# Kernel optimization log

Measured on AMD Instinct MI355X. Metric: run time of the kernel, lower is better.

The kernel has to match this reference:

```python
import jax, jax.numpy as jnp
import numpy as np

HIP_L, HIP_R = 11, 12          # hip joint indices along V
K_LIST = (2, 3, 4, 5)          # soft-selector kNN MoE k values
TAU = 0.35                     # tau_center for ball softmax
EPS = 1e-6


def _sym_norm(A):
    # D^{-1/2} A D^{-1/2} without materializing diag matrices
    d = A.sum(-1)
    dis = jax.lax.rsqrt(d + EPS)
    return dis[..., :, None] * A * dis[..., None, :]


def _knn_adj(pos, k):
    # pos: (N, M, 3) -> 0/1 kNN adjacency (+I self loop, diag ends up 2 as in torch ref)
    M = pos.shape[1]
    diff = pos[:, :, None, :] - pos[:, None, :, :]
    d = jnp.sqrt(jnp.sum(diff * diff, axis=-1))  # (N, M, M) euclidean cdist
    idx = jax.lax.top_k(-d, k)[1]                # (N, M, k) k smallest distances (incl. self)
    A = jax.nn.one_hot(idx, M, dtype=pos.dtype).sum(2)  # scatter 1.0 at kNN columns
    return A + jnp.eye(M, dtype=pos.dtype)


def setup_inputs() -> dict:
    key = jax.random.key(0)
    k1, k2 = jax.random.split(key)
    N, C, T, V, M = 64, 8, 300, 17, 12
    x = jax.random.normal(k1, (N, C, T, V, M), jnp.float32)
    alpha_logits = jax.random.normal(k2, (len(K_LIST),), jnp.float32) * 0.1
    lambda_fuse = jnp.array([0.1], jnp.float32)
    tag_gate = jnp.array([1.0], jnp.float32)
    return {"x": x, "alpha_logits": alpha_logits,
            "lambda_fuse": lambda_fuse, "tag_gate": tag_gate}


def reference(x, alpha_logits, lambda_fuse, tag_gate):
    N, C, T, V, M = x.shape
    # hip-root position averaged over time: (N, M, 3)
    root3 = 0.5 * (x[:, 0:3, :, HIP_L, :] + x[:, 0:3, :, HIP_R, :])  # (N,3,T,M)
    pos = root3.mean(2).transpose(0, 2, 1)                           # (N,M,3)

    # kNN mixture-of-graphs, sym-normalized, detached (detach_adj=True)
    A_knn_stack = jnp.stack([_sym_norm(_knn_adj(pos, k)) for k in K_LIST], 1)  # (N,K,M,M)
    A_knn_stack = jax.lax.stop_gradient(A_knn_stack)
    alpha = jax.nn.softmax(alpha_logits)          # global selector, temp=1
    A_knn = jnp.einsum('k,nkij->nij', alpha, A_knn_stack)

    # soft ball-star graph
    s = x[:, 3].mean((1, 2))                      # (N,M) ball score
    p = jax.nn.softmax(s / TAU, axis=1)
    A_ball = p[:, :, None] + p[:, None, :] + jnp.eye(M, dtype=x.dtype)
    A_ball = jax.lax.stop_gradient(_sym_norm(A_ball))

    # adaptive ball weight from confidence of p (NOT detached)
    w = jnp.clip((jnp.max(p, 1, keepdims=True) - 1.0 / M) / (1.0 - 1.0 / M + EPS), 0.0, 1.0)
    A = w[:, :, None] * A_ball + (1.0 - w[:, :, None]) * A_knn  # (N,M,M)

    # message passing across persons on hip-root features, fused back residually
    root = 0.5 * (x[:, :, :, HIP_L, :] + x[:, :, :, HIP_R, :])  # (N,C,T,M)
    agg = jnp.einsum('nuv,nctv->nctu', A, root)                 # (N,C,T,M)
    g = jnp.tanh(tag_gate[0])  # ramp=1 (ramp_epochs=0), gate_max=1
    return x + g * lambda_fuse[0] * (agg - root)[:, :, :, None, :]
```

## Files before the change

### kernel.cpp

```cpp
#include <hip/hip_runtime.h>
#include <math.h>

#define N_ 64
#define C_ 8
#define T_ 300
#define V_ 17
#define M_ 12
#define EPSF 1e-6f
#define TAUF 0.35f


#define TSPLIT 10
#define TCH (T_ / TSPLIT)

__global__ __launch_bounds__(256) void k_reduce(const float* __restrict__ x,
                                                float* __restrict__ ws_pos,
                                                float* __restrict__ ws_s) {
    const int n = blockIdx.x;
    const int t0 = blockIdx.y * TCH;
    const int tid = threadIdx.x;
    __shared__ float pos_acc[36];
    __shared__ float s_acc[12];
    if (tid < 36) pos_acc[tid] = 0.f;
    if (tid < 12) s_acc[tid] = 0.f;
    __syncthreads();

    {
        const float* xs = x + ((size_t)(n * C_ + 3) * T_ + t0) * 204;
        float a0 = 0.f, a1 = 0.f, a2 = 0.f;
        for (int e = tid; e < TCH * 204; e += 768) {
            a0 += xs[e];
            if (e + 256 < TCH * 204) a1 += xs[e + 256];
            if (e + 512 < TCH * 204) a2 += xs[e + 512];
        }
        int m0 = tid % 12;
        atomicAdd(&s_acc[m0], a0);
        atomicAdd(&s_acc[(m0 + 4) % 12], a1);
        atomicAdd(&s_acc[(m0 + 8) % 12], a2);
    }

    for (int e = tid; e < 3 * TCH * 24; e += 256) {
        int d = e / (TCH * 24);
        int rem = e % (TCH * 24);
        int tt = rem / 24, j = rem % 24;
        float val = x[((size_t)(n * C_ + d) * T_ + t0 + tt) * 204 + 132 + j];
        atomicAdd(&pos_acc[d * 12 + (j % 12)], val);
    }
    __syncthreads();

    if (tid < 36) atomicAdd(&ws_pos[n * 36 + tid], pos_acc[tid]);
    if (tid < 12) atomicAdd(&ws_s[n * 12 + tid], s_acc[tid]);
}

__global__ __launch_bounds__(64) void k_adj(const float* __restrict__ ws_pos,
                                            const float* __restrict__ ws_s,
                                            const float* __restrict__ alpha_logits,
                                            float* __restrict__ ws_A) {
    const int n = blockIdx.x;
    const int tid = threadIdx.x;
    __shared__ float posx[12], posy[12], posz[12];
    __shared__ float dist[144];
    __shared__ int ord[60];
    __shared__ float p_s[12];
    __shared__ float alpha_s[4];
    __shared__ float w_s;

    const float PSC = 0.5f / (float)T_;
    if (tid < 12) {
        posx[tid] = ws_pos[n * 36 + 0 * 12 + tid] * PSC;
        posy[tid] = ws_pos[n * 36 + 1 * 12 + tid] * PSC;
        posz[tid] = ws_pos[n * 36 + 2 * 12 + tid] * PSC;
    }
    if (tid == 0) {
        float l0 = alpha_logits[0], l1 = alpha_logits[1], l2 = alpha_logits[2], l3 = alpha_logits[3];
        float mx = fmaxf(fmaxf(l0, l1), fmaxf(l2, l3));
        float e0 = expf(l0 - mx), e1 = expf(l1 - mx), e2 = expf(l2 - mx), e3 = expf(l3 - mx);
        float s = e0 + e1 + e2 + e3;
        alpha_s[0] = e0 / s; alpha_s[1] = e1 / s; alpha_s[2] = e2 / s; alpha_s[3] = e3 / s;
    }
    if (tid == 1) {
        const float SSC = 1.f / (float)(T_ * V_);
        float sv[12];
        float mx = -1e30f;
        #pragma unroll
        for (int m = 0; m < 12; ++m) { sv[m] = (ws_s[n * 12 + m] * SSC) * (1.f / TAUF); mx = fmaxf(mx, sv[m]); }
        float sum = 0.f;
        #pragma unroll
        for (int m = 0; m < 12; ++m) { sv[m] = expf(sv[m] - mx); sum += sv[m]; }
        float maxp = 0.f;
        #pragma unroll
        for (int m = 0; m < 12; ++m) { sv[m] = sv[m] / sum; p_s[m] = sv[m]; maxp = fmaxf(maxp, sv[m]); }
        float w = (maxp - 1.f / 12.f) / (1.f - 1.f / 12.f + EPSF);
        w_s = fminf(fmaxf(w, 0.f), 1.f);
    }
    __syncthreads();

    for (int e = tid; e < 144; e += 64) {
        int i = e / 12, j = e % 12;
        float dx = posx[i] - posx[j], dy = posy[i] - posy[j], dz = posz[i] - posz[j];
        dist[e] = sqrtf(dx * dx + dy * dy + dz * dz);
    }
    __syncthreads();

    if (tid < 12) {
        int i = tid, mask = 0;
        #pragma unroll
        for (int r = 0; r < 5; ++r) {
            float bd = 1e30f; int bj = -1;
            #pragma unroll
            for (int j = 0; j < 12; ++j) {
                if (!((mask >> j) & 1)) {
                    float dd = dist[i * 12 + j];
                    if (dd < bd) { bd = dd; bj = j; }
                }
            }
            ord[i * 5 + r] = bj; mask |= (1 << bj);
        }
    }
    __syncthreads();

    float w = w_s;
    for (int e = tid; e < 144; e += 64) {
        int i = e / 12, j = e % 12;
        int rank = 5;
        #pragma unroll
        for (int r = 4; r >= 0; --r) if (ord[i * 5 + r] == j) rank = r;
        float diag = (i == j) ? 1.f : 0.f;
        float aknn = 0.f;
        #pragma unroll
        for (int kk = 0; kk < 4; ++kk) {
            int K = kk + 2;
            float val = ((rank < K) ? 1.f : 0.f) + diag;
            aknn += alpha_s[kk] * val / ((float)(K + 1) + EPSF);
        }
        float pi = p_s[i], pj = p_s[j];
        float di = 12.f * pi + 2.f, dj = 12.f * pj + 2.f;
        float ab = (pi + pj + diag) * rsqrtf(di + EPSF) * rsqrtf(dj + EPSF);
        ws_A[n * 144 + e] = w * ab + (1.f - w) * aknn;
    }
}

#define RT 30
__global__ __launch_bounds__(256) void k_main(const float* __restrict__ x,
                                              const float* __restrict__ ws_A,
                                              const float* __restrict__ lambda_fuse,
                                              const float* __restrict__ tag_gate,
                                              float* __restrict__ out) {
    const int n = blockIdx.y;
    const int r0 = blockIdx.x * RT;
    const int tid = threadIdx.x;
    __shared__ float Ash[144];
    __shared__ float root_sh[RT * 12];
    __shared__ float delta_sh[RT * 12];

    if (tid < 144) Ash[tid] = ws_A[n * 144 + tid];
    float scale = tanhf(tag_gate[0]) * lambda_fuse[0];

    const float* xn = x + (size_t)n * 2400 * 204;
    float* on = out + (size_t)n * 2400 * 204;

    for (int e = tid; e < RT * 12; e += 256) {
        int r = e / 12, v = e % 12;
        const float* row = xn + (size_t)(r0 + r) * 204;
        root_sh[e] = 0.5f * (row[132 + v] + row[144 + v]);
    }
    __syncthreads();
    for (int e = tid; e < RT * 12; e += 256) {
        int r = e / 12, u = e % 12;
        float acc = 0.f;
        #pragma unroll
        for (int v = 0; v < 12; ++v) acc += Ash[u * 12 + v] * root_sh[r * 12 + v];
        delta_sh[e] = scale * (acc - root_sh[e]);
    }
    __syncthreads();

    const float4* x4 = (const float4*)(xn + (size_t)r0 * 204);
    float4* o4 = (float4*)(on + (size_t)r0 * 204);
    for (int f = tid; f < RT * 51; f += 256) {
        int r = f / 51, j = f % 51;
        int m0 = (4 * j) % 12;
        float4 v = x4[(size_t)r * 51 + j];
        const float* d = &delta_sh[r * 12 + m0];
        v.x += d[0]; v.y += d[1]; v.z += d[2]; v.w += d[3];
        o4[(size_t)r * 51 + j] = v;
    }
}

extern "C" void kernel_launch(void* const* d_in, const int* in_sizes, int n_in,
                              void* d_out, int out_size, void* d_ws, size_t ws_size,
                              hipStream_t stream) {
    const float* x = (const float*)d_in[0];
    const float* alpha_logits = (const float*)d_in[1];
    const float* lambda_fuse = (const float*)d_in[2];
    const float* tag_gate = (const float*)d_in[3];
    float* out = (float*)d_out;

    float* ws = (float*)d_ws;
    float* ws_pos = ws;
    float* ws_s = ws + 64 * 36;
    float* ws_A = ws + 64 * 48;

    hipMemsetAsync(ws, 0, (size_t)(64 * 48) * sizeof(float), stream);

    k_reduce<<<dim3(N_, TSPLIT), dim3(256), 0, stream>>>(x, ws_pos, ws_s);
    k_adj<<<dim3(N_), dim3(64), 0, stream>>>(ws_pos, ws_s, alpha_logits, ws_A);
    k_main<<<dim3(2400 / RT, N_), dim3(256), 0, stream>>>(x, ws_A, lambda_fuse, tag_gate, out);
}
```

Measured before the change: 255.6 us.

## Drop memset via per-block partial slots; stage x tile in LDS with nontemporal stores

Result: no change. 250.8 us (-1.9%).

```diff
diff --git a/kernel.cpp b/kernel.cpp
--- a/kernel.cpp
+++ b/kernel.cpp
@@ -9,15 +9,17 @@
 #define EPSF 1e-6f
 #define TAUF 0.35f
 
+typedef float f32x4 __attribute__((ext_vector_type(4)));
+
 
 #define TSPLIT 10
 #define TCH (T_ / TSPLIT)
 
 __global__ __launch_bounds__(256) void k_reduce(const float* __restrict__ x,
-                                                float* __restrict__ ws_pos,
-                                                float* __restrict__ ws_s) {
+                                                float* __restrict__ ws_part) {
     const int n = blockIdx.x;
-    const int t0 = blockIdx.y * TCH;
+    const int by = blockIdx.y;
+    const int t0 = by * TCH;
     const int tid = threadIdx.x;
     __shared__ float pos_acc[36];
     __shared__ float s_acc[12];
@@ -48,16 +50,17 @@
     }
     __syncthreads();
 
-    if (tid < 36) atomicAdd(&ws_pos[n * 36 + tid], pos_acc[tid]);
-    if (tid < 12) atomicAdd(&ws_s[n * 12 + tid], s_acc[tid]);
-}
-
-__global__ __launch_bounds__(64) void k_adj(const float* __restrict__ ws_pos,
-                                            const float* __restrict__ ws_s,
+    float* slot = ws_part + (size_t)(n * TSPLIT + by) * 48;
+    if (tid < 36) slot[tid] = pos_acc[tid];
+    if (tid < 12) slot[36 + tid] = s_acc[tid];
+}
+
+__global__ __launch_bounds__(64) void k_adj(const float* __restrict__ ws_part,
                                             const float* __restrict__ alpha_logits,
                                             float* __restrict__ ws_A) {
     const int n = blockIdx.x;
     const int tid = threadIdx.x;
+    __shared__ float raw[48];
     __shared__ float posx[12], posy[12], posz[12];
     __shared__ float dist[144];
     __shared__ int ord[60];
@@ -65,11 +68,19 @@
     __shared__ float alpha_s[4];
     __shared__ float w_s;
 
+    if (tid < 48) {
+        float a = 0.f;
+        #pragma unroll
+        for (int j = 0; j < TSPLIT; ++j) a += ws_part[(size_t)(n * TSPLIT + j) * 48 + tid];
+        raw[tid] = a;
+    }
+    __syncthreads();
+
     const float PSC = 0.5f / (float)T_;
     if (tid < 12) {
-        posx[tid] = ws_pos[n * 36 + 0 * 12 + tid] * PSC;
-        posy[tid] = ws_pos[n * 36 + 1 * 12 + tid] * PSC;
-        posz[tid] = ws_pos[n * 36 + 2 * 12 + tid] * PSC;
+        posx[tid] = raw[0 * 12 + tid] * PSC;
+        posy[tid] = raw[1 * 12 + tid] * PSC;
+        posz[tid] = raw[2 * 12 + tid] * PSC;
     }
     if (tid == 0) {
         float l0 = alpha_logits[0], l1 = alpha_logits[1], l2 = alpha_logits[2], l3 = alpha_logits[3];
@@ -79,11 +90,11 @@
         alpha_s[0] = e0 / s; alpha_s[1] = e1 / s; alpha_s[2] = e2 / s; alpha_s[3] = e3 / s;
     }
     if (tid == 1) {
-        const float SSC = 1.f / (float)(T_ * V_);
+        const float SSC = 1.f / ((float)(T_ * V_) * TAUF);
         float sv[12];
         float mx = -1e30f;
         #pragma unroll
-        for (int m = 0; m < 12; ++m) { sv[m] = (ws_s[n * 12 + m] * SSC) * (1.f / TAUF); mx = fmaxf(mx, sv[m]); }
+        for (int m = 0; m < 12; ++m) { sv[m] = raw[36 + m] * SSC; mx = fmaxf(mx, sv[m]); }
         float sum = 0.f;
         #pragma unroll
         for (int m = 0; m < 12; ++m) { sv[m] = expf(sv[m] - mx); sum += sv[m]; }
@@ -149,20 +160,26 @@
     const int n = blockIdx.y;
     const int r0 = blockIdx.x * RT;
     const int tid = threadIdx.x;
+    __shared__ f32x4 xs4[RT * 51];
     __shared__ float Ash[144];
     __shared__ float root_sh[RT * 12];
     __shared__ float delta_sh[RT * 12];
+    float* xs = (float*)xs4;
 
     if (tid < 144) Ash[tid] = ws_A[n * 144 + tid];
     float scale = tanhf(tag_gate[0]) * lambda_fuse[0];
 
     const float* xn = x + (size_t)n * 2400 * 204;
     float* on = out + (size_t)n * 2400 * 204;
+    const f32x4* x4 = (const f32x4*)(xn + (size_t)r0 * 204);
+    f32x4* o4 = (f32x4*)(on + (size_t)r0 * 204);
+
+    for (int f = tid; f < RT * 51; f += 256) xs4[f] = x4[f];
+    __syncthreads();
 
     for (int e = tid; e < RT * 12; e += 256) {
         int r = e / 12, v = e % 12;
-        const float* row = xn + (size_t)(r0 + r) * 204;
-        root_sh[e] = 0.5f * (row[132 + v] + row[144 + v]);
+        root_sh[e] = 0.5f * (xs[r * 204 + 132 + v] + xs[r * 204 + 144 + v]);
     }
     __syncthreads();
     for (int e = tid; e < RT * 12; e += 256) {
@@ -174,15 +191,13 @@
     }
     __syncthreads();
 
-    const float4* x4 = (const float4*)(xn + (size_t)r0 * 204);
-    float4* o4 = (float4*)(on + (size_t)r0 * 204);
     for (int f = tid; f < RT * 51; f += 256) {
         int r = f / 51, j = f % 51;
         int m0 = (4 * j) % 12;
-        float4 v = x4[(size_t)r * 51 + j];
+        f32x4 v = xs4[f];
         const float* d = &delta_sh[r * 12 + m0];
         v.x += d[0]; v.y += d[1]; v.z += d[2]; v.w += d[3];
-        o4[(size_t)r * 51 + j] = v;
+        __builtin_nontemporal_store(v, &o4[f]);
     }
 }
 
@@ -196,13 +211,10 @@
     float* out = (float*)d_out;
 
     float* ws = (float*)d_ws;
-    float* ws_pos = ws;
-    float* ws_s = ws + 64 * 36;
-    float* ws_A = ws + 64 * 48;
-
-    hipMemsetAsync(ws, 0, (size_t)(64 * 48) * sizeof(float), stream);
-
-    k_reduce<<<dim3(N_, TSPLIT), dim3(256), 0, stream>>>(x, ws_pos, ws_s);
-    k_adj<<<dim3(N_), dim3(64), 0, stream>>>(ws_pos, ws_s, alpha_logits, ws_A);
+    float* ws_part = ws;
+    float* ws_A = ws + 64 * TSPLIT * 48;
+
+    k_reduce<<<dim3(N_, TSPLIT), dim3(256), 0, stream>>>(x, ws_part);
+    k_adj<<<dim3(N_), dim3(64), 0, stream>>>(ws_part, alpha_logits, ws_A);
     k_main<<<dim3(2400 / RT, N_), dim3(256), 0, stream>>>(x, ws_A, lambda_fuse, tag_gate, out);
 }
```
